# Optimization experiments

Measured on AMD Instinct MI355X. Metric: run time of the kernel, lower is better.

## Reference

```python
import jax, jax.numpy as jnp
import numpy as np

D_IN, D_OUT, N_EXP, D_HID = 1024, 1024, 8, 2048
N_TOK = 4096


def setup_inputs() -> dict:
    key = jax.random.key(0)
    ks = jax.random.split(key, 8)
    s_in = 1.0 / np.sqrt(D_IN)
    s_hid = 1.0 / np.sqrt(D_HID)
    s_out = 1.0 / np.sqrt(D_OUT)
    return {
        "x": jax.random.normal(ks[0], (N_TOK, D_IN), dtype=jnp.float32),
        # per-expert MLP weights, stacked along expert axis
        "W1": jax.random.uniform(ks[1], (N_EXP, D_IN, D_HID), jnp.float32, -s_in, s_in),
        "b1": jax.random.uniform(ks[2], (N_EXP, D_HID), jnp.float32, -s_in, s_in),
        "W2": jax.random.uniform(ks[3], (N_EXP, D_HID, D_OUT), jnp.float32, -s_hid, s_hid),
        "b2": jax.random.uniform(ks[4], (N_EXP, D_OUT), jnp.float32, -s_hid, s_hid),
        # shared final linear
        "Wf": jax.random.uniform(ks[5], (D_OUT, D_OUT), jnp.float32, -s_out, s_out),
        "bf": jax.random.uniform(ks[6], (D_OUT,), jnp.float32, -s_out, s_out),
    }


def reference(x, W1, b1, W2, b2, Wf, bf):
    # All experts applied to the same x: batched (grouped) GEMMs via einsum.
    h = jax.nn.relu(jnp.einsum("nd,edh->neh", x, W1) + b1[None])     # [N, E, H]
    y = jnp.einsum("neh,eho->neo", h, W2) + b2[None]                  # [N, E, O]
    z = jnp.einsum("neo,op->nep", y, Wf) + bf                         # shared final linear
    out = jnp.mean(z, axis=1)                                         # mean over experts
    return (out, 0)
```

## Files before the change

### kernel.cpp

```cpp
#include <hip/hip_runtime.h>
#include <hip/hip_bf16.h>


#define D_IN  1024
#define D_HID 2048
#define D_OUT 1024
#define N_EXP 8
#define N_TOK 4096

typedef __attribute__((ext_vector_type(4))) float  f32x4;
typedef __attribute__((ext_vector_type(8))) short  s16x8;
typedef __attribute__((ext_vector_type(4))) short  s16x4;
typedef __attribute__((ext_vector_type(8))) __bf16 b16x8;

static __device__ __forceinline__ f32x4 mfma16x16x32(s16x8 a, s16x8 b, f32x4 c) {
  return __builtin_amdgcn_mfma_f32_16x16x32_bf16(
      __builtin_bit_cast(b16x8, a), __builtin_bit_cast(b16x8, b), c, 0, 0, 0);
}

#define GLDS16(gptr, lptr)                                                         \
  __builtin_amdgcn_global_load_lds(                                               \
      (const __attribute__((address_space(1))) void*)(gptr),                      \
      (__attribute__((address_space(3))) void*)(lptr), 16, 0, 0)

static __device__ __forceinline__ short f2b(float f) {
  return __builtin_bit_cast(short, __float2bfloat16(f));
}
static __device__ __forceinline__ float b2f(short s) {
  return __bfloat162float(__builtin_bit_cast(__hip_bfloat16, s));
}


__global__ void cast_x_kernel(const float* __restrict__ in, short* __restrict__ out, int n4) {
  int i = blockIdx.x * blockDim.x + threadIdx.x;
  if (i >= n4) return;
  f32x4 v = ((const f32x4*)in)[i];
  s16x4 o;
  o[0] = f2b(v[0]); o[1] = f2b(v[1]); o[2] = f2b(v[2]); o[3] = f2b(v[3]);
  ((s16x4*)out)[i] = o;
}

__global__ void tcast_kernel(const float* __restrict__ in, short* __restrict__ out, int R, int C) {
  __shared__ float t[32][33];
  size_t slab = (size_t)blockIdx.z * R * C;
  const float* src = in + slab;
  short* dst = out + slab;
  int c0 = blockIdx.x * 32, r0 = blockIdx.y * 32;
  int tx = threadIdx.x, ty = threadIdx.y;
#pragma unroll
  for (int i = 0; i < 32; i += 8)
    t[ty + i][tx] = src[(size_t)(r0 + ty + i) * C + c0 + tx];
  __syncthreads();
#pragma unroll
  for (int i = 0; i < 32; i += 8)
    dst[(size_t)(c0 + ty + i) * R + r0 + tx] = f2b(t[tx][ty + i]);
}

__global__ void b2mean_kernel(const float* __restrict__ b2, float* __restrict__ b2m) {
  int o = blockIdx.x * blockDim.x + threadIdx.x;
  if (o < D_OUT) {
    float s = 0.f;
#pragma unroll
    for (int e = 0; e < N_EXP; ++e) s += b2[e * D_OUT + o];
    b2m[o] = s * 0.125f;
  }
}


static __device__ __forceinline__ void stage_tile256(
    const short* __restrict__ Ab, const short* __restrict__ Bb, int K, size_t ko,
    short* slotA, short* slotB, int wid, int gr, int gcol) {
#pragma unroll
  for (int r = 0; r < 4; ++r)
    GLDS16(Ab + (size_t)(r * 64 + wid * 8 + gr) * K + ko + gcol,
           slotA + (r * 64 + wid * 8) * 64);
#pragma unroll
  for (int r = 0; r < 4; ++r)
    GLDS16(Bb + (size_t)(r * 64 + wid * 8 + gr) * K + ko + gcol,
           slotB + (r * 64 + wid * 8) * 64);
}

template <bool RELU, bool OUTBF16>
__global__ __launch_bounds__(512) void gemm256_bt_kernel(
    const short* __restrict__ A, const short* __restrict__ Bt, void* __restrict__ C,
    const float* __restrict__ bias, int K, int ldc,
    long sAe, long sBe, long sCe, long sBiasE) {
  constexpr int BM = 256, BN = 256, BK = 64;
  constexpr int SLOT = BM * BK;
  extern __shared__ short lds[];

  const int tid  = threadIdx.x;
  const int wid  = tid >> 6;
  const int lane = tid & 63;
  const int e    = blockIdx.z;

  const short* Ab = A + (size_t)e * sAe + (size_t)blockIdx.y * BM * K;
  const short* Bb = Bt + (size_t)e * sBe + (size_t)blockIdx.x * BN * K;

  const int gr = lane >> 3, gcol = (lane & 7) * 8;
  const int wm = wid >> 2, wn = wid & 3;
  const int lr = lane & 15, lk = (lane >> 4) * 8;

  f32x4 acc[8][4] = {};
  const int nkt = K / BK;

  stage_tile256(Ab, Bb, K, 0, lds, lds + SLOT, wid, gr, gcol);
  __syncthreads();

  for (int kt = 0; kt < nkt; ++kt) {
    const int cur = kt & 1;
    short* curbase = lds + cur * (2 * SLOT);
    short* nxtbase = lds + (cur ^ 1) * (2 * SLOT);

    if (kt + 1 < nkt)
      stage_tile256(Ab, Bb, K, (size_t)(kt + 1) * BK, nxtbase, nxtbase + SLOT,
                    wid, gr, gcol);

    const short* As_ = curbase;
    const short* Bs_ = curbase + SLOT;
#pragma unroll
    for (int ks = 0; ks < 2; ++ks) {
      s16x8 av[8], bv[4];
#pragma unroll
      for (int mi = 0; mi < 8; ++mi)
        av[mi] = *(const s16x8*)&As_[(wm * 128 + mi * 16 + lr) * BK + ks * 32 + lk];
#pragma unroll
      for (int ni = 0; ni < 4; ++ni)
        bv[ni] = *(const s16x8*)&Bs_[(wn * 64 + ni * 16 + lr) * BK + ks * 32 + lk];
#pragma unroll
      for (int mi = 0; mi < 8; ++mi)
#pragma unroll
        for (int ni = 0; ni < 4; ++ni)
          acc[mi][ni] = mfma16x16x32(av[mi], bv[ni], acc[mi][ni]);
    }
    __syncthreads();
  }

  const size_t Cbase = (size_t)e * sCe;
  const int row0 = blockIdx.y * BM + wm * 128 + (lane >> 4) * 4;
  const int col0 = blockIdx.x * BN + wn * 64 + lr;
#pragma unroll
  for (int ni = 0; ni < 4; ++ni) {
    const int col = col0 + ni * 16;
    const float bvv = bias ? bias[(size_t)e * sBiasE + col] : 0.f;
#pragma unroll
    for (int mi = 0; mi < 8; ++mi) {
#pragma unroll
      for (int j = 0; j < 4; ++j) {
        float v = acc[mi][ni][j] + bvv;
        if (RELU) v = v > 0.f ? v : 0.f;
        const size_t idx = Cbase + (size_t)(row0 + mi * 16 + j) * ldc + col;
        if (OUTBF16) ((short*)C)[idx] = f2b(v);
        else         ((float*)C)[idx] = v;
      }
    }
  }
}


template <bool RELU, bool OUTBF16>
__global__ __launch_bounds__(256) void gemm_bt_kernel(
    const short* __restrict__ A, const short* __restrict__ Bt, void* __restrict__ C,
    const float* __restrict__ bias, int K, int ldc,
    long sAe, long sBe, long sCe, long sBiasE) {
  constexpr int BM = 128, BN = 128, BK = 32;
  __shared__ short As[BM * BK];
  __shared__ short Bs[BN * BK];
  const int tid  = threadIdx.x;
  const int wid  = tid >> 6;
  const int lane = tid & 63;
  const int e    = blockIdx.z;

  const short* Ap = A + (size_t)e * sAe + (size_t)blockIdx.y * BM * K;
  const short* Bp = Bt + (size_t)e * sBe + (size_t)blockIdx.x * BN * K;

  const int srow = wid * 16 + (lane >> 2);
  const int scol = (lane & 3) * 8;
  const int wm = (wid >> 1) * 64, wn = (wid & 1) * 64;
  const int lr = lane & 15, lk = (lane >> 4) * 8;

  f32x4 acc[4][4] = {};
  const int nkt = K / BK;
  for (int kt = 0; kt < nkt; ++kt) {
    __syncthreads();
    const size_t ko = (size_t)kt * BK;
    GLDS16(Ap + (size_t)srow * K + ko + scol,        &As[wid * 512]);
    GLDS16(Ap + (size_t)(srow + 64) * K + ko + scol, &As[2048 + wid * 512]);
    GLDS16(Bp + (size_t)srow * K + ko + scol,        &Bs[wid * 512]);
    GLDS16(Bp + (size_t)(srow + 64) * K + ko + scol, &Bs[2048 + wid * 512]);
    __syncthreads();

    s16x8 a[4], b[4];
#pragma unroll
    for (int mi = 0; mi < 4; ++mi)
      a[mi] = *(const s16x8*)&As[(wm + mi * 16 + lr) * BK + lk];
#pragma unroll
    for (int ni = 0; ni < 4; ++ni)
      b[ni] = *(const s16x8*)&Bs[(wn + ni * 16 + lr) * BK + lk];
#pragma unroll
    for (int mi = 0; mi < 4; ++mi)
#pragma unroll
      for (int ni = 0; ni < 4; ++ni)
        acc[mi][ni] = mfma16x16x32(a[mi], b[ni], acc[mi][ni]);
  }

  const size_t Cbase = (size_t)e * sCe;
  const int row0 = blockIdx.y * BM + wm + (lane >> 4) * 4;
  const int col0 = blockIdx.x * BN + wn + lr;
#pragma unroll
  for (int ni = 0; ni < 4; ++ni) {
    const int col = col0 + ni * 16;
    const float bv = bias ? bias[(size_t)e * sBiasE + col] : 0.f;
#pragma unroll
    for (int mi = 0; mi < 4; ++mi) {
#pragma unroll
      for (int j = 0; j < 4; ++j) {
        float v = acc[mi][ni][j] + bv;
        if (RELU) v = v > 0.f ? v : 0.f;
        const size_t idx = Cbase + (size_t)(row0 + mi * 16 + j) * ldc + col;
        if (OUTBF16) ((short*)C)[idx] = f2b(v);
        else         ((float*)C)[idx] = v;
      }
    }
  }
}


__global__ void reduce_y_kernel(const short* __restrict__ yal, const float* __restrict__ b2m,
                                short* __restrict__ ybar, long slab, long total) {
  const size_t base = ((size_t)blockIdx.x * blockDim.x + threadIdx.x) * 8;
  if (base >= (size_t)total) return;
  float s[8] = {};
#pragma unroll
  for (int e = 0; e < N_EXP; ++e) {
    s16x8 v = *(const s16x8*)&yal[(size_t)e * slab + base];
#pragma unroll
    for (int j = 0; j < 8; ++j) s[j] += b2f(v[j]);
  }
  const int col = (int)(base & (D_OUT - 1));
  s16x8 o;
#pragma unroll
  for (int j = 0; j < 8; ++j) o[j] = f2b(s[j] * 0.125f + b2m[col + j]);
  *(s16x8*)&ybar[base] = o;
}

__global__ void tail_kernel(float* __restrict__ out, int from, int n) {
  int i = from + blockIdx.x * blockDim.x + threadIdx.x;
  if (i < n) out[i] = 0.f;
}


extern "C" void kernel_launch(void* const* d_in, const int* in_sizes, int n_in,
                              void* d_out, int out_size, void* d_ws, size_t ws_size,
                              hipStream_t stream) {
  const float* x  = (const float*)d_in[0];
  const float* W1 = (const float*)d_in[1];
  const float* b1 = (const float*)d_in[2];
  const float* W2 = (const float*)d_in[3];
  const float* b2 = (const float*)d_in[4];
  const float* Wf = (const float*)d_in[5];
  const float* bf = (const float*)d_in[6];
  float* out = (float*)d_out;

  const size_t sz_xb  = (size_t)N_TOK * D_IN * 2;
  const size_t sz_W1t = (size_t)N_EXP * D_HID * D_IN * 2;
  const size_t sz_W2t = (size_t)N_EXP * D_OUT * D_HID * 2;
  const size_t sz_Wft = (size_t)D_OUT * D_OUT * 2;
  const size_t sz_b2m = (size_t)D_OUT * 4;
  const size_t sz_ybr = (size_t)N_TOK * D_OUT * 2;
  const size_t fixed  = sz_xb + sz_W1t + sz_W2t + sz_Wft + sz_b2m + sz_ybr;
  const size_t per_full = (size_t)N_EXP * N_TOK * D_HID * 2
                        + (size_t)N_EXP * N_TOK * D_OUT * 2;
  int NC = 16;
  for (int c = 1; c <= 8; c <<= 1) {
    if (fixed + per_full / c <= ws_size) { NC = c; break; }
  }
  const int ntokc = N_TOK / NC;

  char* ws = (char*)d_ws;
  short* xb  = (short*)ws; ws += sz_xb;
  short* W1t = (short*)ws; ws += sz_W1t;
  short* W2t = (short*)ws; ws += sz_W2t;
  short* Wft = (short*)ws; ws += sz_Wft;
  float* b2m = (float*)ws; ws += sz_b2m;
  short* ybr = (short*)ws; ws += sz_ybr;
  short* h   = (short*)ws; ws += (size_t)N_EXP * ntokc * D_HID * 2;
  short* yal = (short*)ws;

  hipLaunchKernelGGL(cast_x_kernel, dim3(N_TOK * D_IN / 4 / 256), dim3(256), 0, stream,
                     x, xb, N_TOK * D_IN / 4);
  hipLaunchKernelGGL(tcast_kernel, dim3(D_HID / 32, D_IN / 32, N_EXP), dim3(32, 8), 0, stream,
                     W1, W1t, D_IN, D_HID);
  hipLaunchKernelGGL(tcast_kernel, dim3(D_OUT / 32, D_HID / 32, N_EXP), dim3(32, 8), 0, stream,
                     W2, W2t, D_HID, D_OUT);
  hipLaunchKernelGGL(tcast_kernel, dim3(D_OUT / 32, D_OUT / 32, 1), dim3(32, 8), 0, stream,
                     Wf, Wft, D_OUT, D_OUT);
  hipLaunchKernelGGL(b2mean_kernel, dim3(4), dim3(256), 0, stream, b2, b2m);

  const size_t ldsz = 131072;

  for (int c = 0; c < NC; ++c) {
    const short* xc = xb + (size_t)c * ntokc * D_IN;
    short* ybc = ybr + (size_t)c * ntokc * D_OUT;

    hipLaunchKernelGGL((gemm256_bt_kernel<true, true>),
                       dim3(D_HID / 256, ntokc / 256, N_EXP), dim3(512), ldsz, stream,
                       xc, W1t, (void*)h, b1, D_IN, D_HID,
                       0L, (long)D_HID * D_IN, (long)ntokc * D_HID, (long)D_HID);

    hipLaunchKernelGGL((gemm256_bt_kernel<false, true>),
                       dim3(D_OUT / 256, ntokc / 256, N_EXP), dim3(512), ldsz, stream,
                       h, W2t, (void*)yal, (const float*)nullptr, D_HID, D_OUT,
                       (long)ntokc * D_HID, (long)D_OUT * D_HID, (long)ntokc * D_OUT, 0L);

    hipLaunchKernelGGL(reduce_y_kernel, dim3(ntokc * D_OUT / 8 / 256), dim3(256), 0, stream,
                       yal, b2m, ybc, (long)ntokc * D_OUT, (long)ntokc * D_OUT);
  }

  hipLaunchKernelGGL((gemm_bt_kernel<false, false>),
                     dim3(D_OUT / 128, N_TOK / 128, 1), dim3(256), 0, stream,
                     ybr, Wft, d_out, bf, D_OUT, D_OUT, 0L, 0L, 0L, 0L);

  int tail = out_size - N_TOK * D_OUT;
  if (tail > 0)
    hipLaunchKernelGGL(tail_kernel, dim3((tail + 63) / 64), dim3(64), 0, stream,
                       out, N_TOK * D_OUT, out_size);
}
```

Baseline: 422.4 us.

## Replace double-buffered K loop with 4-slot ring pipeline using BK=32

The 256x256 expert GEMM now streams K in 32-wide tiles through a 4-slot LDS ring, keeping three tiles in flight. It waits on partial vmcnt counts with a single barrier per step, replacing the full-drain double buffer. MFMA issue runs at raised wave priority. This aims to hide global-to-LDS latency and cut barrier stalls, at the cost of more loop iterations and hand-tuned waitcnt accounting that must match the number of loads issued per stage.

Result: faster. 413.7 us (-2.1%).

```diff
diff --git a/kernel.cpp b/kernel.cpp
--- a/kernel.cpp
+++ b/kernel.cpp
@@ -22,6 +22,14 @@
   __builtin_amdgcn_global_load_lds(                                               \
       (const __attribute__((address_space(1))) void*)(gptr),                      \
       (__attribute__((address_space(3))) void*)(lptr), 16, 0, 0)
+
+#define WAITV(n) asm volatile("s_waitcnt vmcnt(" #n ")" ::: "memory")
+#define SBAR()                                                                     \
+  do {                                                                             \
+    __builtin_amdgcn_sched_barrier(0);                                             \
+    __builtin_amdgcn_s_barrier();                                                  \
+    __builtin_amdgcn_sched_barrier(0);                                             \
+  } while (0)
 
 static __device__ __forceinline__ short f2b(float f) {
   return __builtin_bit_cast(short, __float2bfloat16(f));
@@ -67,26 +75,13 @@
 }
 
 
-static __device__ __forceinline__ void stage_tile256(
-    const short* __restrict__ Ab, const short* __restrict__ Bb, int K, size_t ko,
-    short* slotA, short* slotB, int wid, int gr, int gcol) {
-#pragma unroll
-  for (int r = 0; r < 4; ++r)
-    GLDS16(Ab + (size_t)(r * 64 + wid * 8 + gr) * K + ko + gcol,
-           slotA + (r * 64 + wid * 8) * 64);
-#pragma unroll
-  for (int r = 0; r < 4; ++r)
-    GLDS16(Bb + (size_t)(r * 64 + wid * 8 + gr) * K + ko + gcol,
-           slotB + (r * 64 + wid * 8) * 64);
-}
-
 template <bool RELU, bool OUTBF16>
-__global__ __launch_bounds__(512) void gemm256_bt_kernel(
+__global__ __launch_bounds__(512) void gemm256_ring_kernel(
     const short* __restrict__ A, const short* __restrict__ Bt, void* __restrict__ C,
     const float* __restrict__ bias, int K, int ldc,
     long sAe, long sBe, long sCe, long sBiasE) {
-  constexpr int BM = 256, BN = 256, BK = 64;
-  constexpr int SLOT = BM * BK;
+  constexpr int BM = 256, BN = 256, BK = 32;
+  constexpr int SLOT = 16384;
   extern __shared__ short lds[];
 
   const int tid  = threadIdx.x;
@@ -97,44 +92,60 @@
   const short* Ab = A + (size_t)e * sAe + (size_t)blockIdx.y * BM * K;
   const short* Bb = Bt + (size_t)e * sBe + (size_t)blockIdx.x * BN * K;
 
-  const int gr = lane >> 3, gcol = (lane & 7) * 8;
+  const int strow = wid * 16 + (lane >> 2);
+  const int stcol = (lane & 3) * 8;
+
   const int wm = wid >> 2, wn = wid & 3;
   const int lr = lane & 15, lk = (lane >> 4) * 8;
 
   f32x4 acc[8][4] = {};
   const int nkt = K / BK;
 
-  stage_tile256(Ab, Bb, K, 0, lds, lds + SLOT, wid, gr, gcol);
-  __syncthreads();
-
-  for (int kt = 0; kt < nkt; ++kt) {
-    const int cur = kt & 1;
-    short* curbase = lds + cur * (2 * SLOT);
-    short* nxtbase = lds + (cur ^ 1) * (2 * SLOT);
-
-    if (kt + 1 < nkt)
-      stage_tile256(Ab, Bb, K, (size_t)(kt + 1) * BK, nxtbase, nxtbase + SLOT,
-                    wid, gr, gcol);
-
-    const short* As_ = curbase;
-    const short* Bs_ = curbase + SLOT;
-#pragma unroll
-    for (int ks = 0; ks < 2; ++ks) {
-      s16x8 av[8], bv[4];
-#pragma unroll
-      for (int mi = 0; mi < 8; ++mi)
-        av[mi] = *(const s16x8*)&As_[(wm * 128 + mi * 16 + lr) * BK + ks * 32 + lk];
+  auto STAGE = [&](int t) {
+    short* slot = lds + (size_t)(t & 3) * SLOT;
+    const size_t ko = (size_t)t * BK;
+#pragma unroll
+    for (int r = 0; r < 2; ++r) {
+      GLDS16(Ab + (size_t)(r * 128 + strow) * K + ko + stcol,
+             slot + r * 4096 + wid * 512);
+      GLDS16(Bb + (size_t)(r * 128 + strow) * K + ko + stcol,
+             slot + 8192 + r * 4096 + wid * 512);
+    }
+  };
+
+  auto COMPUTE = [&](int t) {
+    const short* As_ = lds + (size_t)(t & 3) * SLOT;
+    const short* Bs_ = As_ + 8192;
+    s16x8 av[8], bv[4];
+#pragma unroll
+    for (int mi = 0; mi < 8; ++mi)
+      av[mi] = *(const s16x8*)&As_[(wm * 128 + mi * 16 + lr) * BK + lk];
+#pragma unroll
+    for (int ni = 0; ni < 4; ++ni)
+      bv[ni] = *(const s16x8*)&Bs_[(wn * 64 + ni * 16 + lr) * BK + lk];
+    __builtin_amdgcn_s_setprio(1);
+#pragma unroll
+    for (int mi = 0; mi < 8; ++mi)
 #pragma unroll
       for (int ni = 0; ni < 4; ++ni)
-        bv[ni] = *(const s16x8*)&Bs_[(wn * 64 + ni * 16 + lr) * BK + ks * 32 + lk];
-#pragma unroll
-      for (int mi = 0; mi < 8; ++mi)
-#pragma unroll
-        for (int ni = 0; ni < 4; ++ni)
-          acc[mi][ni] = mfma16x16x32(av[mi], bv[ni], acc[mi][ni]);
-    }
-    __syncthreads();
-  }
+        acc[mi][ni] = mfma16x16x32(av[mi], bv[ni], acc[mi][ni]);
+    __builtin_amdgcn_s_setprio(0);
+  };
+
+  STAGE(0); STAGE(1); STAGE(2);
+
+  for (int t = 0; t < nkt - 2; ++t) {
+    WAITV(8);
+    SBAR();
+    if (t + 3 < nkt) STAGE(t + 3);
+    COMPUTE(t);
+  }
+  WAITV(4);
+  SBAR();
+  COMPUTE(nkt - 2);
+  WAITV(0);
+  SBAR();
+  COMPUTE(nkt - 1);
 
   const size_t Cbase = (size_t)e * sCe;
   const int row0 = blockIdx.y * BM + wm * 128 + (lane >> 4) * 4;
@@ -303,12 +314,12 @@
     const short* xc = xb + (size_t)c * ntokc * D_IN;
     short* ybc = ybr + (size_t)c * ntokc * D_OUT;
 
-    hipLaunchKernelGGL((gemm256_bt_kernel<true, true>),
+    hipLaunchKernelGGL((gemm256_ring_kernel<true, true>),
                        dim3(D_HID / 256, ntokc / 256, N_EXP), dim3(512), ldsz, stream,
                        xc, W1t, (void*)h, b1, D_IN, D_HID,
                        0L, (long)D_HID * D_IN, (long)ntokc * D_HID, (long)D_HID);
 
-    hipLaunchKernelGGL((gemm256_bt_kernel<false, true>),
+    hipLaunchKernelGGL((gemm256_ring_kernel<false, true>),
                        dim3(D_OUT / 256, ntokc / 256, N_EXP), dim3(512), ldsz, stream,
                        h, W2t, (void*)yal, (const float*)nullptr, D_HID, D_OUT,
                        (long)ntokc * D_HID, (long)D_OUT * D_HID, (long)ntokc * D_OUT, 0L);
```
